# Optimization experiments

Measured on AMD Instinct MI355X. Metric: run time of the kernel, lower is better.

## Reference

```python
import jax, jax.numpy as jnp
import numpy as np

G = 8          # offset_groups (= heads)
HEADS = 8
DH = 64        # dim_head
DS = 4         # downsample_factor (also offset_scale)


def gconv1x1(x, w, g):
    # grouped 1x1 conv; w: (cout, cin//g, 1, 1) torch layout
    b, cin, H, W = x.shape
    cout = w.shape[0]
    xg = x.reshape(b, g, cin // g, H, W)
    wg = w[:, :, 0, 0].reshape(g, cout // g, cin // g)
    y = jnp.einsum('bgihw,goi->bgohw', xg, wg)
    return y.reshape(b, cout, H, W)


def grid_sample_bilinear_zeros(img, grid):
    # img: (N,C,H,W); grid: (N,Hg,Wg,2) with last dim (x,y) in [-1,1], align_corners=False
    N, C, H, W = img.shape
    Hg, Wg = grid.shape[1:3]
    x = (grid[..., 0] + 1.0) * (W / 2.0) - 0.5
    y = (grid[..., 1] + 1.0) * (H / 2.0) - 0.5
    x0 = jnp.floor(x); y0 = jnp.floor(y)
    wx1 = x - x0; wx0 = 1.0 - wx1
    wy1 = y - y0; wy0 = 1.0 - wy1
    x0i = x0.astype(jnp.int32); x1i = x0i + 1
    y0i = y0.astype(jnp.int32); y1i = y0i + 1
    img_flat = img.reshape(N, C, H * W)

    def gather(yi, xi):
        valid = ((yi >= 0) & (yi < H) & (xi >= 0) & (xi < W)).astype(img.dtype)
        idx = jnp.clip(yi, 0, H - 1) * W + jnp.clip(xi, 0, W - 1)
        v = jnp.take_along_axis(img_flat, idx.reshape(N, 1, Hg * Wg), axis=2)
        return v.reshape(N, C, Hg, Wg) * valid[:, None]

    return (gather(y0i, x0i) * (wy0 * wx0)[:, None]
            + gather(y0i, x1i) * (wy0 * wx1)[:, None]
            + gather(y1i, x0i) * (wy1 * wx0)[:, None]
            + gather(y1i, x1i) * (wy1 * wx1)[:, None])


def _forward(x, q_w, k_w, v_w, out_w, out_b, off_w1, off_b1, off_w2,
             cpb_w1, cpb_b1, cpb_w2, cpb_b2, cpb_w3, cpb_b3):
    b, dim, H, W = x.shape
    q = gconv1x1(x, q_w, G)                       # (b, 512, H, W)
    gq = q.reshape(b * G, -1, H, W)               # 'b (g d) ... -> (b g) d ...'
    # offset net: depthwise 6x6 stride-4 conv -> GELU -> 1x1 -> tanh -> *scale
    off = jax.lax.conv_general_dilated(gq, off_w1, (DS, DS), ((1, 1), (1, 1)),
                                       dimension_numbers=('NCHW', 'OIHW', 'NCHW'),
                                       feature_group_count=off_w1.shape[0])
    off = jax.nn.gelu(off + off_b1[None, :, None, None], approximate=False)
    off = jnp.einsum('bchw,oc->bohw', off, off_w2[:, :, 0, 0])
    off = jnp.tanh(off) * float(DS)               # offset_scale = downsample_factor
    h2, w2 = off.shape[-2:]
    gx, gy = jnp.meshgrid(jnp.arange(w2), jnp.arange(h2), indexing='xy')
    grid = jnp.stack([gx, gy], 0).astype(off.dtype)  # (2,h2,w2): ch0=x, ch1=y
    vgrid = grid[None] + off                         # (b*G, 2, h2, w2)
    # normalize_grid (faithful to original: ch0 normed by h2-1, ch1 by w2-1)
    g0 = 2.0 * vgrid[:, 0] / max(h2 - 1, 1) - 1.0
    g1 = 2.0 * vgrid[:, 1] / max(w2 - 1, 1) - 1.0
    vgrid_scaled = jnp.stack([g0, g1], -1)           # (b*G, h2, w2, 2)
    gx_img = x.reshape(b * G, dim // G, H, W)
    kv = grid_sample_bilinear_zeros(gx_img, vgrid_scaled)
    kv = kv.reshape(b, dim, h2, w2)
    k = gconv1x1(kv, k_w, G)
    v = gconv1x1(kv, v_w, G)
    i = H * W; j = h2 * w2
    scale = DH ** -0.5
    qh = (q * scale).reshape(b, HEADS, DH, i).transpose(0, 1, 3, 2)  # (b,h,i,d)
    kh = k.reshape(b, HEADS, DH, j).transpose(0, 1, 3, 2)
    vh = v.reshape(b, HEADS, DH, j).transpose(0, 1, 3, 2)
    sim = jnp.einsum('bhid,bhjd->bhij', qh, kh)
    # CPB relative position bias
    qx, qy = jnp.meshgrid(jnp.arange(W), jnp.arange(H), indexing='xy')
    grid_q = jnp.stack([2.0 * qx / max(H - 1, 1) - 1.0,
                        2.0 * qy / max(W - 1, 1) - 1.0], -1).astype(x.dtype)
    grid_q = grid_q.reshape(1, i, 2)
    grid_kv = vgrid_scaled.reshape(b * G, j, 2)
    pos = grid_q[:, :, None, :] - grid_kv[:, None, :, :]   # (b*G, i, j, 2)
    cb = jnp.sign(pos) * jnp.log1p(jnp.abs(pos))
    cb = jax.nn.relu(cb @ cpb_w1.T + cpb_b1)
    cb = jax.nn.relu(cb @ cpb_w2.T + cpb_b2)
    cb = cb @ cpb_w3.T + cpb_b3                             # (b*G, i, j, o)
    o = cpb_w3.shape[0]
    bias = cb.reshape(b, G, i, j, o).transpose(0, 1, 4, 2, 3).reshape(b, G * o, i, j)
    sim = sim + bias
    sim = sim - jax.lax.stop_gradient(jnp.max(sim, axis=-1, keepdims=True))
    attn = jax.nn.softmax(sim, axis=-1)
    out = jnp.einsum('bhij,bhjd->bhid', attn, vh)
    out = out.transpose(0, 1, 3, 2).reshape(b, HEADS * DH, H, W)
    out = jnp.einsum('bchw,oc->bohw', out, out_w[:, :, 0, 0]) + out_b[None, :, None, None]
    return out


def setup_inputs() -> dict:
    key = jax.random.key(0)
    ks = jax.random.split(key, 16)
    dim, inner = 256, HEADS * DH  # 256, 512
    n = lambda k, shp, s=0.05: (s * jax.random.normal(k, shp)).astype(jnp.float32)
    return {
        'x': jax.random.normal(ks[0], (2, dim, 32, 32), dtype=jnp.float32),
        'q_w': n(ks[1], (inner, dim // G, 1, 1)),
        'k_w': n(ks[2], (inner, dim // G, 1, 1)),
        'v_w': n(ks[3], (inner, dim // G, 1, 1)),
        'out_w': n(ks[4], (dim, inner, 1, 1)),
        'out_b': n(ks[5], (dim,), 0.01),
        'off_w1': n(ks[6], (inner // G, 1, 6, 6)),
        'off_b1': n(ks[7], (inner // G,), 0.01),
        'off_w2': n(ks[8], (2, inner // G, 1, 1)),
        'cpb_w1': n(ks[9], (dim // 4, 2), 0.2),
        'cpb_b1': n(ks[10], (dim // 4,), 0.01),
        'cpb_w2': n(ks[11], (dim // 4, dim // 4), 0.1),
        'cpb_b2': n(ks[12], (dim // 4,), 0.01),
        'cpb_w3': n(ks[13], (HEADS // G, dim // 4), 0.1),
        'cpb_b3': n(ks[14], (HEADS // G,), 0.01),
    }


def reference(x, q_w, k_w, v_w, out_w, out_b, off_w1, off_b1, off_w2,
              cpb_w1, cpb_b1, cpb_w2, cpb_b2, cpb_w3, cpb_b3):
    return _forward(x, q_w, k_w, v_w, out_w, out_b, off_w1, off_b1, off_w2,
                    cpb_w1, cpb_b1, cpb_w2, cpb_b2, cpb_w3, cpb_b3)
```

## Files before the change

kernel.cpp:

```cpp
#include <hip/hip_runtime.h>
#include <math.h>

#define NPX 1024

using bf16x8 = __attribute__((ext_vector_type(8))) short;
using f32x4  = __attribute__((ext_vector_type(4))) float;
using u32x4  = __attribute__((ext_vector_type(4))) unsigned;

__device__ __forceinline__ float fast_slog1p(float p) {
  return copysignf(__logf(1.f + fabsf(p)), p);
}

__device__ __forceinline__ unsigned short f2bf(float f) {
  unsigned u = __builtin_bit_cast(unsigned, f);
  unsigned r = (u + 0x7FFFu + ((u >> 16) & 1u)) >> 16;
  return (unsigned short)r;
}
__device__ __forceinline__ float bf2f(unsigned short h) {
  return __builtin_bit_cast(float, (unsigned)h << 16);
}
__device__ __forceinline__ unsigned cvt_pk(float lo, float hi) {
  unsigned r;
  asm("v_cvt_pk_bf16_f32 %0, %1, %2" : "=v"(r) : "v"(lo), "v"(hi));
  return r;
}

__global__ __launch_bounds__(256) void k_prep_w(const float* __restrict__ ow,
                                                const float* __restrict__ w2g,
                                                unsigned short* __restrict__ whP,
                                                unsigned short* __restrict__ wlP,
                                                unsigned short* __restrict__ w2P) {
  if (blockIdx.x < 512) {
    int idx = blockIdx.x * 256 + threadIdx.x;
    int o = idx >> 9, c = idx & 511;
    float v = ow[(size_t)o * 512 + c];
    unsigned short hi = f2bf(v);
    unsigned short lo = f2bf(v - bf2f(hi));
    int kt = c >> 5, lg = (c >> 3) & 3, r = c & 7;
    size_t dst = ((size_t)(kt * 4 + lg) * 256 + o) * 8 + r;
    whP[dst] = hi;
    wlP[dst] = lo;
  } else {
    for (int e = threadIdx.x; e < 4096; e += 256) {
      int r = e & 7;
      int f = (e >> 3) & 7;
      int c2t = f >> 1, s = f & 1;
      int lane = e >> 6;
      int lm = lane & 15, lg = lane >> 4;
      int c2 = c2t * 16 + lm, c = s * 32 + lg * 8 + r;
      w2P[e] = f2bf(w2g[c2 * 64 + c]);
    }
  }
}

__global__ __launch_bounds__(256) void k_qconv(const float* __restrict__ x,
                                               const float* __restrict__ qw,
                                               float* __restrict__ q,
                                               float* __restrict__ qT) {
  const int blk = blockIdx.x;
  const int bg  = blk >> 4;
  const int px0 = (blk & 15) << 6;
  const int g   = bg & 7;
  const int b   = bg >> 3;
  const int tid = threadIdx.x;
  __shared__ float xs[32 * 64];
  __shared__ float wsh[64 * 32];
  __shared__ float ot[64 * 65];

  const float* xb = x + ((size_t)(b * 256 + g * 32)) * NPX + px0;
  for (int idx = tid; idx < 32 * 64; idx += 256) {
    int c = idx >> 6, p = idx & 63;
    xs[idx] = xb[(size_t)c * NPX + p];
  }
  const float* wb = qw + g * 64 * 32;
  for (int idx = tid; idx < 64 * 32; idx += 256) wsh[idx] = wb[idx];
  __syncthreads();

  for (int idx = tid; idx < 64 * 64; idx += 256) {
    int o = idx >> 6, p = idx & 63;
    float a0 = 0.f, a1 = 0.f;
#pragma unroll
    for (int c = 0; c < 32; c += 2) {
      a0 = fmaf(wsh[o * 32 + c],     xs[c * 64 + p],       a0);
      a1 = fmaf(wsh[o * 32 + c + 1], xs[(c + 1) * 64 + p], a1);
    }
    float acc = a0 + a1;
    q[((size_t)(bg * 64 + o)) * NPX + px0 + p] = acc;
    ot[o * 65 + p] = acc * 0.125f;
  }
  __syncthreads();
  float* qTb = qT + ((size_t)bg * NPX + px0) * 64;
  for (int idx = tid; idx < 64 * 64; idx += 256) {
    int p = idx >> 6, o = idx & 63;
    qTb[p * 64 + o] = ot[o * 65 + p];
  }
}

__global__ __launch_bounds__(256) void k_offset_sample(
    const float* __restrict__ q, const float* __restrict__ w1,
    const float* __restrict__ b1, const float* __restrict__ w2,
    const float* __restrict__ x, const float* __restrict__ kw,
    const float* __restrict__ vw, float* __restrict__ gkv,
    float* __restrict__ kh,
    unsigned short* __restrict__ vPh, unsigned short* __restrict__ vPl) {
  const int px0 = blockIdx.x << 3;
  const int bg  = blockIdx.y;
  const int g   = bg & 7;
  const int tid = threadIdx.x;
  __shared__ float ge[64 * 9];
  __shared__ float w1s[64 * 36];
  __shared__ float b1s[64];
  __shared__ float kws[64 * 33];
  __shared__ float vws[64 * 33];
  __shared__ float smp[32 * 9];
  __shared__ float xs_[8], ys_[8];

  for (int idx = tid; idx < 64 * 36; idx += 256) w1s[idx] = w1[idx];
  if (tid < 64) b1s[tid] = b1[tid];
  for (int idx = tid; idx < 2048; idx += 256) {
    int o = idx >> 5, c = idx & 31;
    kws[o * 33 + c] = kw[(g * 64 + o) * 32 + c];
    vws[o * 33 + c] = vw[(g * 64 + o) * 32 + c];
  }
  __syncthreads();

  const float* qb = q + (size_t)bg * 64 * NPX;
  for (int idx = tid; idx < 512; idx += 256) {
    int c = idx >> 3, lp = idx & 7;
    int px = px0 + lp;
    int oy = px >> 3, ox = px & 7;
    const float* qc = qb + (size_t)c * NPX;
    float acc = 0.f;
#pragma unroll
    for (int ky = 0; ky < 6; ++ky) {
      int yy = oy * 4 - 1 + ky;
      if (yy < 0 || yy >= 32) continue;
#pragma unroll
      for (int kx = 0; kx < 6; ++kx) {
        int xx = ox * 4 - 1 + kx;
        if (xx < 0 || xx >= 32) continue;
        acc = fmaf(w1s[c * 36 + ky * 6 + kx], qc[yy * 32 + xx], acc);
      }
    }
    acc += b1s[c];
    ge[c * 9 + lp] = 0.5f * acc * (1.f + erff(acc * 0.70710678118654752440f));
  }
  __syncthreads();

  {
    int lp = tid >> 5, sl = tid & 31;
    float s0 = 0.f, s1 = 0.f;
#pragma unroll
    for (int k = 0; k < 2; ++k) {
      int c = sl + k * 32;
      float gv = ge[c * 9 + lp];
      s0 = fmaf(w2[c],      gv, s0);
      s1 = fmaf(w2[64 + c], gv, s1);
    }
#pragma unroll
    for (int off = 16; off > 0; off >>= 1) {
      s0 += __shfl_xor(s0, off, 32);
      s1 += __shfl_xor(s1, off, 32);
    }
    if (sl == 0) {
      float o0 = tanhf(s0) * 4.f;
      float o1 = tanhf(s1) * 4.f;
      int px = px0 + lp;
      int oy = px >> 3, ox = px & 7;
      float g0 = 2.f * ((float)ox + o0) / 7.f - 1.f;
      float g1 = 2.f * ((float)oy + o1) / 7.f - 1.f;
      gkv[(bg * 64 + px) * 2 + 0] = g0;
      gkv[(bg * 64 + px) * 2 + 1] = g1;
      xs_[lp] = (g0 + 1.f) * 16.f - 0.5f;
      ys_[lp] = (g1 + 1.f) * 16.f - 0.5f;
    }
  }
  __syncthreads();

  const float* imgb = x + (size_t)bg * 32 * NPX;
  for (int idx = tid; idx < 256; idx += 256) {
    int c = idx >> 3, lj = idx & 7;
    float xx = xs_[lj], yy = ys_[lj];
    float x0f = floorf(xx), y0f = floorf(yy);
    int x0 = (int)x0f, y0 = (int)y0f;
    float wx1 = xx - x0f, wy1 = yy - y0f;
    float wx0 = 1.f - wx1, wy0 = 1.f - wy1;
    int x1 = x0 + 1, y1 = y0 + 1;
    bool vx0 = (x0 >= 0) & (x0 < 32), vx1 = (x1 >= 0) & (x1 < 32);
    bool vy0 = (y0 >= 0) & (y0 < 32), vy1 = (y1 >= 0) & (y1 < 32);
    int cx0 = min(max(x0, 0), 31), cx1 = min(max(x1, 0), 31);
    int cy0 = min(max(y0, 0), 31), cy1 = min(max(y1, 0), 31);
    const float* img = imgb + (size_t)c * NPX;
    float v00 = (vy0 && vx0) ? img[cy0 * 32 + cx0] : 0.f;
    float v01 = (vy0 && vx1) ? img[cy0 * 32 + cx1] : 0.f;
    float v10 = (vy1 && vx0) ? img[cy1 * 32 + cx0] : 0.f;
    float v11 = (vy1 && vx1) ? img[cy1 * 32 + cx1] : 0.f;
    smp[c * 9 + lj] = v00 * wy0 * wx0 + v01 * wy0 * wx1 +
                      v10 * wy1 * wx0 + v11 * wy1 * wx1;
  }
  __syncthreads();

  for (int idx = tid; idx < 512; idx += 256) {
    int lj = idx >> 6, o = idx & 63;
    int j = px0 + lj;
    float ak0 = 0.f, ak1 = 0.f, av0 = 0.f, av1 = 0.f;
#pragma unroll
    for (int c = 0; c < 32; c += 2) {
      float s0 = smp[c * 9 + lj], s1 = smp[(c + 1) * 9 + lj];
      ak0 = fmaf(kws[o * 33 + c],     s0, ak0);
      ak1 = fmaf(kws[o * 33 + c + 1], s1, ak1);
      av0 = fmaf(vws[o * 33 + c],     s0, av0);
      av1 = fmaf(vws[o * 33 + c + 1], s1, av1);
    }
    kh[((size_t)bg * 64 + j) * 64 + o] = ak0 + ak1;
    float av = av0 + av1;
    unsigned short hi = f2bf(av);
    unsigned short lo = f2bf(av - bf2f(hi));
    int s  = (j >> 5) & 1, lgj = (j >> 3) & 3, r = j & 7;
    int nb = o >> 4, lmo = o & 15;
    size_t dst = (((size_t)(bg * 4 + nb) * 64) + lgj * 16 + lmo) * 16 + s * 8 + r;
    vPh[dst] = hi;
    vPl[dst] = lo;
  }
}

__global__ __launch_bounds__(256) void k_attn(
    const float* __restrict__ qT, const float* __restrict__ kh,
    const unsigned short* __restrict__ vPh, const unsigned short* __restrict__ vPl,
    const float* __restrict__ gkv,
    const float* __restrict__ w1, const float* __restrict__ b1,
    const unsigned short* __restrict__ w2P, const float* __restrict__ b2,
    const float* __restrict__ w3, const float* __restrict__ b3,
    unsigned short* __restrict__ aoh, unsigned short* __restrict__ aol) {
  const int it  = blockIdx.x;
  const int bh  = blockIdx.y;
  const int i0  = it << 4;
  const int iy  = i0 >> 5;
  const int ixb = i0 & 31;
  const int tid = threadIdx.x;

  __shared__ float utab[16 * 65];
  __shared__ float vtab[64];
  __shared__ float w1xs[64], w1ys[64], b1s[64], b2s[64], w3s[64];
  __shared__ float sim[16 * 65];

  const int w  = tid >> 6;
  const int l  = tid & 63;
  const int lm = l & 15;
  const int lg = l >> 4;
  const int jb = w * 16;

  bf16x8 bw2[4][2];
  {
    const unsigned short* wp = w2P + (lg * 16 + lm) * 64;
#pragma unroll
    for (int c2t = 0; c2t < 4; ++c2t)
#pragma unroll
      for (int s = 0; s < 2; ++s)
        bw2[c2t][s] = *(const bf16x8*)(wp + (c2t * 2 + s) * 8);
  }
  bf16x8 bvh[2], bvl[2];
  {
    const size_t vbase = (((size_t)(bh * 4 + w) * 64) + l) * 16;
#pragma unroll
    for (int s = 0; s < 2; ++s) {
      bvh[s] = *(const bf16x8*)(vPh + vbase + s * 8);
      bvl[s] = *(const bf16x8*)(vPl + vbase + s * 8);
    }
  }

  for (int idx = tid; idx < 1024; idx += 256) {
    int il = idx >> 6, j = idx & 63;
    float kxv = gkv[(bh * 64 + j) * 2];
    float qxn = (2.f / 31.f) * (float)(ixb + il) - 1.f;
    utab[il * 65 + j] = fast_slog1p(qxn - kxv);
  }
  if (tid < 64) {
    w1xs[tid] = w1[tid * 2];
    w1ys[tid] = w1[tid * 2 + 1];
    b1s[tid]  = b1[tid];
    b2s[tid]  = b2[tid];
    w3s[tid]  = w3[tid];
    float kyv = gkv[(bh * 64 + tid) * 2 + 1];
    float qyn = (2.f / 31.f) * (float)iy - 1.f;
    vtab[tid] = fast_slog1p(qyn - kyv);
  }
  __syncthreads();

  float w1v[16], tc[16];
  {
    float vvj = vtab[jb + lm];
#pragma unroll
    for (int s = 0; s < 2; ++s)
#pragma unroll
      for (int r = 0; r < 8; ++r) {
        int c = s * 32 + lg * 8 + r;
        w1v[s * 8 + r] = w1xs[c];
        tc[s * 8 + r]  = fmaf(w1ys[c], vvj, b1s[c]);
      }
  }
  float b2r[4][4], w3r[4][4];
#pragma unroll
  for (int c2t = 0; c2t < 4; ++c2t)
#pragma unroll
    for (int r = 0; r < 4; ++r) {
      int c2 = c2t * 16 + lg * 4 + r;
      b2r[c2t][r] = b2s[c2];
      w3r[c2t][r] = w3s[c2];
    }
  const float b3v = b3[0];

#pragma unroll 2
  for (int il = 0; il < 16; ++il) {
    float u = utab[il * 65 + jb + lm];
    float h[16];
#pragma unroll
    for (int e = 0; e < 16; ++e)
      h[e] = fmaxf(fmaf(w1v[e], u, tc[e]), 0.f);
    bf16x8 hf[2];
#pragma unroll
    for (int s = 0; s < 2; ++s) {
      u32x4 wds;
#pragma unroll
      for (int p = 0; p < 4; ++p)
        wds[p] = cvt_pk(h[s * 8 + p * 2], h[s * 8 + p * 2 + 1]);
      hf[s] = __builtin_bit_cast(bf16x8, wds);
    }
    float tot = 0.f;
#pragma unroll
    for (int c2t = 0; c2t < 4; ++c2t) {
      f32x4 acc = (f32x4){b2r[c2t][0], b2r[c2t][1], b2r[c2t][2], b2r[c2t][3]};
      acc = __builtin_amdgcn_mfma_f32_16x16x32_bf16(bw2[c2t][0], hf[0], acc, 0, 0, 0);
      acc = __builtin_amdgcn_mfma_f32_16x16x32_bf16(bw2[c2t][1], hf[1], acc, 0, 0, 0);
#pragma unroll
      for (int r = 0; r < 4; ++r)
        tot = fmaf(fmaxf(acc[r], 0.f), w3r[c2t][r], tot);
    }
    tot += __shfl_xor(tot, 16);
    tot += __shfl_xor(tot, 32);
    if (lg == 0)
      sim[il * 65 + jb + lm] = tot + b3v;
  }

  {
    bf16x8 aq[2], bk[2];
    const float* qb = qT + ((size_t)bh * NPX + i0 + lm) * 64;
    const float* kb = kh + ((size_t)(bh * 64 + jb + lm)) * 64;
#pragma unroll
    for (int s = 0; s < 2; ++s) {
      float4 q0 = *(const float4*)(qb + s * 32 + lg * 8);
      float4 q1 = *(const float4*)(qb + s * 32 + lg * 8 + 4);
      float4 k0 = *(const float4*)(kb + s * 32 + lg * 8);
      float4 k1 = *(const float4*)(kb + s * 32 + lg * 8 + 4);
      u32x4 wq, wk;
      wq[0] = cvt_pk(q0.x, q0.y); wq[1] = cvt_pk(q0.z, q0.w);
      wq[2] = cvt_pk(q1.x, q1.y); wq[3] = cvt_pk(q1.z, q1.w);
      wk[0] = cvt_pk(k0.x, k0.y); wk[1] = cvt_pk(k0.z, k0.w);
      wk[2] = cvt_pk(k1.x, k1.y); wk[3] = cvt_pk(k1.z, k1.w);
      aq[s] = __builtin_bit_cast(bf16x8, wq);
      bk[s] = __builtin_bit_cast(bf16x8, wk);
    }
    f32x4 qacc = (f32x4){0.f, 0.f, 0.f, 0.f};
    qacc = __builtin_amdgcn_mfma_f32_16x16x32_bf16(aq[0], bk[0], qacc, 0, 0, 0);
    qacc = __builtin_amdgcn_mfma_f32_16x16x32_bf16(aq[1], bk[1], qacc, 0, 0, 0);
#pragma unroll
    for (int r = 0; r < 4; ++r)
      sim[(lg * 4 + r) * 65 + jb + lm] += qacc[r];
  }
  __syncthreads();

  {
    int r = tid >> 4, sl = tid & 15;
    float sv[4];
    float m = -1e30f;
#pragma unroll
    for (int t = 0; t < 4; ++t) {
      sv[t] = sim[r * 65 + sl + (t << 4)];
      m = fmaxf(m, sv[t]);
    }
#pragma unroll
    for (int off = 8; off > 0; off >>= 1) m = fmaxf(m, __shfl_xor(m, off, 16));
    float ssum = 0.f;
#pragma unroll
    for (int t = 0; t < 4; ++t) { sv[t] = expf(sv[t] - m); ssum += sv[t]; }
#pragma unroll
    for (int off = 8; off > 0; off >>= 1) ssum += __shfl_xor(ssum, off, 16);
    float inv = 1.f / ssum;
#pragma unroll
    for (int t = 0; t < 4; ++t) sim[r * 65 + sl + (t << 4)] = sv[t] * inv;
  }
  __syncthreads();

  {
    bf16x8 ap[2];
#pragma unroll
    for (int s = 0; s < 2; ++s) {
      u32x4 wp;
#pragma unroll
      for (int p = 0; p < 4; ++p)
        wp[p] = cvt_pk(sim[lm * 65 + s * 32 + lg * 8 + p * 2],
                       sim[lm * 65 + s * 32 + lg * 8 + p * 2 + 1]);
      ap[s] = __builtin_bit_cast(bf16x8, wp);
    }
    f32x4 po = (f32x4){0.f, 0.f, 0.f, 0.f};
    po = __builtin_amdgcn_mfma_f32_16x16x32_bf16(ap[0], bvh[0], po, 0, 0, 0);
    po = __builtin_amdgcn_mfma_f32_16x16x32_bf16(ap[1], bvh[1], po, 0, 0, 0);
    po = __builtin_amdgcn_mfma_f32_16x16x32_bf16(ap[0], bvl[0], po, 0, 0, 0);
    po = __builtin_amdgcn_mfma_f32_16x16x32_bf16(ap[1], bvl[1], po, 0, 0, 0);
    const int b = bh >> 3, h = bh & 7;
    size_t base = ((size_t)(b * 1024 + i0 + lg * 4)) * 512 + h * 64 + jb + lm;
#pragma unroll
    for (int r = 0; r < 4; ++r) {
      float v = po[r];
      unsigned short hi = f2bf(v);
      aoh[base + (size_t)r * 512] = hi;
      aol[base + (size_t)r * 512] = f2bf(v - bf2f(hi));
    }
  }
}

__global__ __launch_bounds__(256) void k_proj_mfma(
    const unsigned short* __restrict__ aoh, const unsigned short* __restrict__ aol,
    const unsigned short* __restrict__ whP, const unsigned short* __restrict__ wlP,
    const float* __restrict__ ob, float* __restrict__ out) {
  const int p0 = blockIdx.x << 4;
  const int b  = p0 >> 10;
  const int pb = p0 & 1023;
  const int w  = threadIdx.x >> 6;
  const int l  = threadIdx.x & 63;
  const int lm = l & 15, lg = l >> 4;

  f32x4 acc[4];
#pragma unroll
  for (int nt = 0; nt < 4; ++nt) acc[nt] = (f32x4){0.f, 0.f, 0.f, 0.f};

  const unsigned short* arh = aoh + ((size_t)(p0 + lm)) * 512 + lg * 8;
  const unsigned short* arl = aol + ((size_t)(p0 + lm)) * 512 + lg * 8;
  const int ob0 = w * 64;

#pragma unroll 4
  for (int kt = 0; kt < 16; ++kt) {
    bf16x8 ah = *(const bf16x8*)(arh + kt * 32);
    bf16x8 al = *(const bf16x8*)(arl + kt * 32);
    const size_t wb = ((size_t)(kt * 4 + lg) * 256 + ob0 + lm) * 8;
#pragma unroll
    for (int nt = 0; nt < 4; ++nt) {
      bf16x8 bhf = *(const bf16x8*)(whP + wb + nt * 128);
      bf16x8 blf = *(const bf16x8*)(wlP + wb + nt * 128);
      acc[nt] = __builtin_amdgcn_mfma_f32_16x16x32_bf16(ah, bhf, acc[nt], 0, 0, 0);
      acc[nt] = __builtin_amdgcn_mfma_f32_16x16x32_bf16(ah, blf, acc[nt], 0, 0, 0);
      acc[nt] = __builtin_amdgcn_mfma_f32_16x16x32_bf16(al, bhf, acc[nt], 0, 0, 0);
    }
  }
#pragma unroll
  for (int nt = 0; nt < 4; ++nt) {
    int o = ob0 + nt * 16 + lm;
    float bias = ob[o];
    float4 v;
    v.x = acc[nt][0] + bias;
    v.y = acc[nt][1] + bias;
    v.z = acc[nt][2] + bias;
    v.w = acc[nt][3] + bias;
    *(float4*)(out + ((size_t)(b * 256 + o)) * NPX + pb + lg * 4) = v;
  }
}

extern "C" void kernel_launch(void* const* d_in, const int* in_sizes, int n_in,
                              void* d_out, int out_size, void* d_ws, size_t ws_size,
                              hipStream_t stream) {
  const float* x      = (const float*)d_in[0];
  const float* q_w    = (const float*)d_in[1];
  const float* k_w    = (const float*)d_in[2];
  const float* v_w    = (const float*)d_in[3];
  const float* out_w  = (const float*)d_in[4];
  const float* out_b  = (const float*)d_in[5];
  const float* off_w1 = (const float*)d_in[6];
  const float* off_b1 = (const float*)d_in[7];
  const float* off_w2 = (const float*)d_in[8];
  const float* cpb_w1 = (const float*)d_in[9];
  const float* cpb_b1 = (const float*)d_in[10];
  const float* cpb_w2 = (const float*)d_in[11];
  const float* cpb_b2 = (const float*)d_in[12];
  const float* cpb_w3 = (const float*)d_in[13];
  const float* cpb_b3 = (const float*)d_in[14];
  float* out = (float*)d_out;

  float* ws  = (float*)d_ws;
  float* q   = ws;
  unsigned short* aoh = (unsigned short*)q;
  unsigned short* aol = aoh + 2048 * 512;
  float* qT  = ws + 1048576;
  float* kh  = qT + 1048576;
  float* gkv = kh + 65536;
  unsigned short* whP = (unsigned short*)(gkv + 2048);
  unsigned short* wlP = whP + 131072;
  unsigned short* w2P = wlP + 131072;
  unsigned short* vPh = w2P + 4096;
  unsigned short* vPl = vPh + 65536;

  k_prep_w<<<513, 256, 0, stream>>>(out_w, cpb_w2, whP, wlP, w2P);
  k_qconv<<<256, 256, 0, stream>>>(x, q_w, q, qT);
  k_offset_sample<<<dim3(8, 16), 256, 0, stream>>>(q, off_w1, off_b1, off_w2,
                                                   x, k_w, v_w, gkv, kh, vPh, vPl);
  k_attn<<<dim3(64, 16), 256, 0, stream>>>(qT, kh, vPh, vPl, gkv, cpb_w1, cpb_b1,
                                           w2P, cpb_b2, cpb_w3, cpb_b3,
                                           aoh, aol);
  k_proj_mfma<<<128, 256, 0, stream>>>(aoh, aol, whP, wlP, out_b, out);
}
```

Before: 74.15 us.

## Split attention work across two wave groups and halve qconv pixel tiles

k_attn now runs 512 threads per block. Two groups of four waves each handle half of the 16 query rows in the CPB MLP loop and half of the K dimension in the QK and PV MFMAs, then combine partial results through shared memory with extra barriers. k_qconv uses 32-pixel tiles with twice as many blocks. The aim is more parallelism and occupancy per block on a fixed grid, paid for with extra synchronization and shared-memory reductions.

```diff
diff --git a/kernel.cpp b/kernel.cpp
--- a/kernel.cpp
+++ b/kernel.cpp
@@ -58,41 +58,41 @@
                                                float* __restrict__ q,
                                                float* __restrict__ qT) {
   const int blk = blockIdx.x;
-  const int bg  = blk >> 4;
-  const int px0 = (blk & 15) << 6;
+  const int bg  = blk >> 5;
+  const int px0 = (blk & 31) << 5;
   const int g   = bg & 7;
   const int b   = bg >> 3;
   const int tid = threadIdx.x;
-  __shared__ float xs[32 * 64];
+  __shared__ float xs[32 * 32];
   __shared__ float wsh[64 * 32];
-  __shared__ float ot[64 * 65];
+  __shared__ float ot[64 * 33];
 
   const float* xb = x + ((size_t)(b * 256 + g * 32)) * NPX + px0;
-  for (int idx = tid; idx < 32 * 64; idx += 256) {
-    int c = idx >> 6, p = idx & 63;
+  for (int idx = tid; idx < 32 * 32; idx += 256) {
+    int c = idx >> 5, p = idx & 31;
     xs[idx] = xb[(size_t)c * NPX + p];
   }
   const float* wb = qw + g * 64 * 32;
   for (int idx = tid; idx < 64 * 32; idx += 256) wsh[idx] = wb[idx];
   __syncthreads();
 
-  for (int idx = tid; idx < 64 * 64; idx += 256) {
-    int o = idx >> 6, p = idx & 63;
+  for (int idx = tid; idx < 64 * 32; idx += 256) {
+    int o = idx >> 5, p = idx & 31;
     float a0 = 0.f, a1 = 0.f;
 #pragma unroll
     for (int c = 0; c < 32; c += 2) {
-      a0 = fmaf(wsh[o * 32 + c],     xs[c * 64 + p],       a0);
-      a1 = fmaf(wsh[o * 32 + c + 1], xs[(c + 1) * 64 + p], a1);
+      a0 = fmaf(wsh[o * 32 + c],     xs[c * 32 + p],       a0);
+      a1 = fmaf(wsh[o * 32 + c + 1], xs[(c + 1) * 32 + p], a1);
     }
     float acc = a0 + a1;
     q[((size_t)(bg * 64 + o)) * NPX + px0 + p] = acc;
-    ot[o * 65 + p] = acc * 0.125f;
+    ot[o * 33 + p] = acc * 0.125f;
   }
   __syncthreads();
   float* qTb = qT + ((size_t)bg * NPX + px0) * 64;
-  for (int idx = tid; idx < 64 * 64; idx += 256) {
+  for (int idx = tid; idx < 32 * 64; idx += 256) {
     int p = idx >> 6, o = idx & 63;
-    qTb[p * 64 + o] = ot[o * 65 + p];
+    qTb[p * 64 + o] = ot[o * 33 + p];
   }
 }
 
@@ -224,7 +224,7 @@
   }
 }
 
-__global__ __launch_bounds__(256) void k_attn(
+__global__ __launch_bounds__(512) void k_attn(
     const float* __restrict__ qT, const float* __restrict__ kh,
     const unsigned short* __restrict__ vPh, const unsigned short* __restrict__ vPl,
     const float* __restrict__ gkv,
@@ -242,13 +242,16 @@
   __shared__ float utab[16 * 65];
   __shared__ float vtab[64];
   __shared__ float w1xs[64], w1ys[64], b1s[64], b2s[64], w3s[64];
-  __shared__ float sim[16 * 65];
-
-  const int w  = tid >> 6;
-  const int l  = tid & 63;
-  const int lm = l & 15;
-  const int lg = l >> 4;
-  const int jb = w * 16;
+  __shared__ float simA[16 * 65];
+  __shared__ float simB[16 * 65];
+
+  const int wave = tid >> 6;
+  const int wg   = wave >> 2;
+  const int w    = wave & 3;
+  const int l    = tid & 63;
+  const int lm   = l & 15;
+  const int lg   = l >> 4;
+  const int jb   = w * 16;
 
   bf16x8 bw2[4][2];
   {
@@ -259,17 +262,14 @@
       for (int s = 0; s < 2; ++s)
         bw2[c2t][s] = *(const bf16x8*)(wp + (c2t * 2 + s) * 8);
   }
-  bf16x8 bvh[2], bvl[2];
-  {
-    const size_t vbase = (((size_t)(bh * 4 + w) * 64) + l) * 16;
-#pragma unroll
-    for (int s = 0; s < 2; ++s) {
-      bvh[s] = *(const bf16x8*)(vPh + vbase + s * 8);
-      bvl[s] = *(const bf16x8*)(vPl + vbase + s * 8);
-    }
-  }
-
-  for (int idx = tid; idx < 1024; idx += 256) {
+  bf16x8 bvh1, bvl1;
+  {
+    const size_t vbase = (((size_t)(bh * 4 + w) * 64) + l) * 16 + wg * 8;
+    bvh1 = *(const bf16x8*)(vPh + vbase);
+    bvl1 = *(const bf16x8*)(vPl + vbase);
+  }
+
+  for (int idx = tid; idx < 1024; idx += 512) {
     int il = idx >> 6, j = idx & 63;
     float kxv = gkv[(bh * 64 + j) * 2];
     float qxn = (2.f / 31.f) * (float)(ixb + il) - 1.f;
@@ -311,7 +311,8 @@
   const float b3v = b3[0];
 
 #pragma unroll 2
-  for (int il = 0; il < 16; ++il) {
+  for (int ii = 0; ii < 8; ++ii) {
+    int il = wg * 8 + ii;
     float u = utab[il * 65 + jb + lm];
     float h[16];
 #pragma unroll
@@ -339,82 +340,81 @@
     tot += __shfl_xor(tot, 16);
     tot += __shfl_xor(tot, 32);
     if (lg == 0)
-      sim[il * 65 + jb + lm] = tot + b3v;
-  }
-
-  {
-    bf16x8 aq[2], bk[2];
-    const float* qb = qT + ((size_t)bh * NPX + i0 + lm) * 64;
-    const float* kb = kh + ((size_t)(bh * 64 + jb + lm)) * 64;
-#pragma unroll
-    for (int s = 0; s < 2; ++s) {
-      float4 q0 = *(const float4*)(qb + s * 32 + lg * 8);
-      float4 q1 = *(const float4*)(qb + s * 32 + lg * 8 + 4);
-      float4 k0 = *(const float4*)(kb + s * 32 + lg * 8);
-      float4 k1 = *(const float4*)(kb + s * 32 + lg * 8 + 4);
-      u32x4 wq, wk;
-      wq[0] = cvt_pk(q0.x, q0.y); wq[1] = cvt_pk(q0.z, q0.w);
-      wq[2] = cvt_pk(q1.x, q1.y); wq[3] = cvt_pk(q1.z, q1.w);
-      wk[0] = cvt_pk(k0.x, k0.y); wk[1] = cvt_pk(k0.z, k0.w);
-      wk[2] = cvt_pk(k1.x, k1.y); wk[3] = cvt_pk(k1.z, k1.w);
-      aq[s] = __builtin_bit_cast(bf16x8, wq);
-      bk[s] = __builtin_bit_cast(bf16x8, wk);
-    }
+      simA[il * 65 + jb + lm] = tot + b3v;
+  }
+  __syncthreads();
+
+  {
+    const float* qb = qT + ((size_t)bh * NPX + i0 + lm) * 64 + wg * 32;
+    const float* kb = kh + ((size_t)(bh * 64 + jb + lm)) * 64 + wg * 32;
+    float4 q0 = *(const float4*)(qb + lg * 8);
+    float4 q1 = *(const float4*)(qb + lg * 8 + 4);
+    float4 k0 = *(const float4*)(kb + lg * 8);
+    float4 k1 = *(const float4*)(kb + lg * 8 + 4);
+    u32x4 wq, wk;
+    wq[0] = cvt_pk(q0.x, q0.y); wq[1] = cvt_pk(q0.z, q0.w);
+    wq[2] = cvt_pk(q1.x, q1.y); wq[3] = cvt_pk(q1.z, q1.w);
+    wk[0] = cvt_pk(k0.x, k0.y); wk[1] = cvt_pk(k0.z, k0.w);
+    wk[2] = cvt_pk(k1.x, k1.y); wk[3] = cvt_pk(k1.z, k1.w);
+    bf16x8 aq = __builtin_bit_cast(bf16x8, wq);
+    bf16x8 bk = __builtin_bit_cast(bf16x8, wk);
     f32x4 qacc = (f32x4){0.f, 0.f, 0.f, 0.f};
-    qacc = __builtin_amdgcn_mfma_f32_16x16x32_bf16(aq[0], bk[0], qacc, 0, 0, 0);
-    qacc = __builtin_amdgcn_mfma_f32_16x16x32_bf16(aq[1], bk[1], qacc, 0, 0, 0);
-#pragma unroll
-    for (int r = 0; r < 4; ++r)
-      sim[(lg * 4 + r) * 65 + jb + lm] += qacc[r];
-  }
-  __syncthreads();
-
-  {
-    int r = tid >> 4, sl = tid & 15;
-    float sv[4];
-    float m = -1e30f;
-#pragma unroll
-    for (int t = 0; t < 4; ++t) {
-      sv[t] = sim[r * 65 + sl + (t << 4)];
-      m = fmaxf(m, sv[t]);
-    }
-#pragma unroll
-    for (int off = 8; off > 0; off >>= 1) m = fmaxf(m, __shfl_xor(m, off, 16));
-    float ssum = 0.f;
-#pragma unroll
-    for (int t = 0; t < 4; ++t) { sv[t] = expf(sv[t] - m); ssum += sv[t]; }
-#pragma unroll
-    for (int off = 8; off > 0; off >>= 1) ssum += __shfl_xor(ssum, off, 16);
+    qacc = __builtin_amdgcn_mfma_f32_16x16x32_bf16(aq, bk, qacc, 0, 0, 0);
+    if (wg == 0) {
+#pragma unroll
+      for (int r = 0; r < 4; ++r)
+        simA[(lg * 4 + r) * 65 + jb + lm] += qacc[r];
+    } else {
+#pragma unroll
+      for (int r = 0; r < 4; ++r)
+        simB[(lg * 4 + r) * 65 + jb + lm] = qacc[r];
+    }
+  }
+  __syncthreads();
+
+  {
+    int r = tid >> 5, sl = tid & 31;
+    float s0 = simA[r * 65 + sl]      + simB[r * 65 + sl];
+    float s1 = simA[r * 65 + sl + 32] + simB[r * 65 + sl + 32];
+    float m = fmaxf(s0, s1);
+#pragma unroll
+    for (int off = 16; off > 0; off >>= 1) m = fmaxf(m, __shfl_xor(m, off, 32));
+    float e0 = expf(s0 - m), e1 = expf(s1 - m);
+    float ssum = e0 + e1;
+#pragma unroll
+    for (int off = 16; off > 0; off >>= 1) ssum += __shfl_xor(ssum, off, 32);
     float inv = 1.f / ssum;
-#pragma unroll
-    for (int t = 0; t < 4; ++t) sim[r * 65 + sl + (t << 4)] = sv[t] * inv;
-  }
-  __syncthreads();
-
-  {
-    bf16x8 ap[2];
-#pragma unroll
-    for (int s = 0; s < 2; ++s) {
-      u32x4 wp;
-#pragma unroll
-      for (int p = 0; p < 4; ++p)
-        wp[p] = cvt_pk(sim[lm * 65 + s * 32 + lg * 8 + p * 2],
-                       sim[lm * 65 + s * 32 + lg * 8 + p * 2 + 1]);
-      ap[s] = __builtin_bit_cast(bf16x8, wp);
-    }
+    simA[r * 65 + sl]      = e0 * inv;
+    simA[r * 65 + sl + 32] = e1 * inv;
+  }
+  __syncthreads();
+
+  {
+    u32x4 wp;
+#pragma unroll
+    for (int p = 0; p < 4; ++p)
+      wp[p] = cvt_pk(simA[lm * 65 + wg * 32 + lg * 8 + p * 2],
+                     simA[lm * 65 + wg * 32 + lg * 8 + p * 2 + 1]);
+    bf16x8 ap = __builtin_bit_cast(bf16x8, wp);
     f32x4 po = (f32x4){0.f, 0.f, 0.f, 0.f};
-    po = __builtin_amdgcn_mfma_f32_16x16x32_bf16(ap[0], bvh[0], po, 0, 0, 0);
-    po = __builtin_amdgcn_mfma_f32_16x16x32_bf16(ap[1], bvh[1], po, 0, 0, 0);
-    po = __builtin_amdgcn_mfma_f32_16x16x32_bf16(ap[0], bvl[0], po, 0, 0, 0);
-    po = __builtin_amdgcn_mfma_f32_16x16x32_bf16(ap[1], bvl[1], po, 0, 0, 0);
-    const int b = bh >> 3, h = bh & 7;
-    size_t base = ((size_t)(b * 1024 + i0 + lg * 4)) * 512 + h * 64 + jb + lm;
-#pragma unroll
-    for (int r = 0; r < 4; ++r) {
-      float v = po[r];
-      unsigned short hi = f2bf(v);
-      aoh[base + (size_t)r * 512] = hi;
-      aol[base + (size_t)r * 512] = f2bf(v - bf2f(hi));
+    po = __builtin_amdgcn_mfma_f32_16x16x32_bf16(ap, bvh1, po, 0, 0, 0);
+    po = __builtin_amdgcn_mfma_f32_16x16x32_bf16(ap, bvl1, po, 0, 0, 0);
+    if (wg == 1) {
+#pragma unroll
+      for (int r = 0; r < 4; ++r)
+        utab[(lg * 4 + r) * 65 + jb + lm] = po[r];
+    }
+    __syncthreads();
+    if (wg == 0) {
+      const int b = bh >> 3, h = bh & 7;
+      size_t base = ((size_t)(b * 1024 + i0 + lg * 4)) * 512 + h * 64 + jb + lm;
+#pragma unroll
+      for (int r = 0; r < 4; ++r) {
+        float v = po[r] + utab[(lg * 4 + r) * 65 + jb + lm];
+        unsigned short hi = f2bf(v);
+        aoh[base + (size_t)r * 512] = hi;
+        aol[base + (size_t)r * 512] = f2bf(v - bf2f(hi));
+      }
     }
   }
 }
@@ -499,10 +499,10 @@
   unsigned short* vPl = vPh + 65536;
 
   k_prep_w<<<513, 256, 0, stream>>>(out_w, cpb_w2, whP, wlP, w2P);
-  k_qconv<<<256, 256, 0, stream>>>(x, q_w, q, qT);
+  k_qconv<<<512, 256, 0, stream>>>(x, q_w, q, qT);
   k_offset_sample<<<dim3(8, 16), 256, 0, stream>>>(q, off_w1, off_b1, off_w2,
                                                    x, k_w, v_w, gkv, kh, vPh, vPl);
-  k_attn<<<dim3(64, 16), 256, 0, stream>>>(qT, kh, vPh, vPl, gkv, cpb_w1, cpb_b1,
+  k_attn<<<dim3(64, 16), 512, 0, stream>>>(qT, kh, vPh, vPl, gkv, cpb_w1, cpb_b1,
                                            w2P, cpb_b2, cpb_w3, cpb_b3,
                                            aoh, aol);
   k_proj_mfma<<<128, 256, 0, stream>>>(aoh, aol, whP, wlP, out_b, out);
```

New measurement: 80.97 us. 1.09x slower.
